# Kernel optimization log

Hardware: AMD Instinct MI355X
Metric: run time of the kernel (lower is better)

The kernel has to match this reference:

```python
import jax, jax.numpy as jnp
import numpy as np

# --- SOM geometry constants (match init_kwargs) ---
MAP_ROWS, MAP_COLS = 32, 32
N_PROTO = MAP_ROWS * MAP_COLS
SIGMA = 1.0
PBC = True


def _build_neighborhood():
    """Gaussian neighborhood h[i,j]=exp(-dist(i,j)^2/(2*sigma^2)) on a hexagonal
    grid with periodic boundary conditions (faithful to Neighborhoods(...,'Hexagons','grid',PBC=True))."""
    rr, cc = np.meshgrid(np.arange(MAP_ROWS), np.arange(MAP_COLS), indexing='ij')
    # hexagonal lattice coordinates: odd rows shifted by 0.5, row spacing sqrt(3)/2
    x = cc + 0.5 * (rr % 2)
    y = rr * (np.sqrt(3.0) / 2.0)
    pos = np.stack([x.ravel(), y.ravel()], axis=1).astype(np.float64)  # [M, 2]
    diff = pos[:, None, :] - pos[None, :, :]                            # [M, M, 2]
    if PBC:
        width = float(MAP_COLS)
        height = MAP_ROWS * (np.sqrt(3.0) / 2.0)
        d2 = np.full((N_PROTO, N_PROTO), np.inf)
        for sx in (-1.0, 0.0, 1.0):
            for sy in (-1.0, 0.0, 1.0):
                dx = diff[..., 0] + sx * width
                dy = diff[..., 1] + sy * height
                d2 = np.minimum(d2, dx * dx + dy * dy)
    else:
        d2 = (diff ** 2).sum(-1)
    return np.exp(-d2 / (2.0 * SIGMA ** 2)).astype(np.float32)         # [M, M]


H = jnp.asarray(_build_neighborhood())  # constant [M, M] neighborhood matrix


def setup_inputs() -> dict:
    key = jax.random.key(0)
    k1, k2 = jax.random.split(key)
    inputs = jax.random.normal(k1, (16384, 256), dtype=jnp.float32)
    prototypes = jax.random.normal(k2, (N_PROTO, 256), dtype=jnp.float32) * 0.05
    return {"inputs": inputs, "prototypes": prototypes}


def reference(inputs, prototypes):
    # squared euclidean distances d[n, m] = ||x_n - p_m||^2, computed without
    # materializing the (N, M, D) broadcast intermediate
    x2 = jnp.sum(inputs * inputs, axis=1, keepdims=True)        # [N, 1]
    p2 = jnp.sum(prototypes * prototypes, axis=1)               # [M]
    d = x2 - 2.0 * (inputs @ prototypes.T) + p2[None, :]        # [N, M]
    energies = H @ d.T                                          # [M, N]
    bmus = jnp.argmin(energies, axis=0)                         # [N]
    out = 0.5 * jnp.take_along_axis(energies, bmus[None, :], axis=0)  # [1, N]
    return out
```

## Files before the change

### kernel.cpp

```cpp
#include <hip/hip_runtime.h>
#include <hip/hip_bf16.h>
#include <math.h>

#define D 256
#define NPROTO 1024
#define NROWS 16384
#define WRr 13
#define WCc 18
#define WJ (WRr * WCc)
#define JSUB 59
#define GMAT_BLOCKS (NPROTO / 4)
#define XPREP_BLOCKS (NROWS / 32)

#define WAITVM(N) asm volatile("s_waitcnt vmcnt(" #N ")" ::: "memory")

typedef __attribute__((ext_vector_type(8))) short short8;
typedef __attribute__((ext_vector_type(4))) float f32x4;

__device__ __forceinline__ int swz_key(int row) {
    return (row & 3) ^ ((row >> 2) & 3);
}

__device__ __forceinline__ short f2bf(float f) {
    union { __hip_bfloat16 b; short s; } u;
    u.b = __float2bfloat16(f);
    return u.s;
}

__device__ __forceinline__ void gload_lds16(void* lds, const void* g) {
    __builtin_amdgcn_global_load_lds(
        (const __attribute__((address_space(1))) unsigned*)g,
        (__attribute__((address_space(3))) unsigned*)lds, 16, 0, 0);
}

__device__ __forceinline__ void proto_pos(int idx, double& x, double& y) {
    int r = idx >> 5, c = idx & 31;
    x = (double)c + 0.5 * (double)(r & 1);
    y = (double)r * 0.86602540378443864676;
}

__device__ __forceinline__ float hval(int i, int j) {
    double xi, yi, xj, yj;
    proto_pos(i, xi, yi);
    proto_pos(j, xj, yj);
    double dx0 = xi - xj, dy0 = yi - yj;
    const double W = 32.0;
    const double Hh = 27.712812921102035;
    double best = 1e300;
#pragma unroll
    for (int sx = -1; sx <= 1; ++sx) {
        double dx = dx0 + (double)sx * W;
#pragma unroll
        for (int sy = -1; sy <= 1; ++sy) {
            double dy = dy0 + (double)sy * Hh;
            double d2 = dx * dx + dy * dy;
            best = fmin(best, d2);
        }
    }
    return (float)exp(-0.5 * best);
}


__global__ void __launch_bounds__(256) prep_kernel(
    const float* __restrict__ X, const float* __restrict__ P,
    short* __restrict__ XgS, short* __restrict__ GbS,
    float* __restrict__ x2, float* __restrict__ hsum, float* __restrict__ hp2,
    unsigned* __restrict__ out) {
    int t = threadIdx.x;
    int bx = blockIdx.x;

    if (bx >= GMAT_BLOCKS) {
        int base0 = (bx - GMAT_BLOCKS) * 32;
        int g = t & 31;
        int kt = g >> 2;
        int slot = g & 3;
#pragma unroll
        for (int it = 0; it < 4; ++it) {
            int row = base0 + it * 8 + (t >> 5);
            const float4* src = reinterpret_cast<const float4*>(X + (size_t)row * D) + g * 2;
            float4 a = src[0], b = src[1];
            float s = a.x * a.x + a.y * a.y + a.z * a.z + a.w * a.w +
                      b.x * b.x + b.y * b.y + b.z * b.z + b.w * b.w;
            s += __shfl_xor(s, 1);
            s += __shfl_xor(s, 2);
            s += __shfl_xor(s, 4);
            s += __shfl_xor(s, 8);
            s += __shfl_xor(s, 16);
            if (g == 0) x2[row] = s;
            short8 w;
            w[0] = f2bf(a.x); w[1] = f2bf(a.y); w[2] = f2bf(a.z); w[3] = f2bf(a.w);
            w[4] = f2bf(b.x); w[5] = f2bf(b.y); w[6] = f2bf(b.z); w[7] = f2bf(b.w);
            *reinterpret_cast<short8*>(
                XgS + (size_t)kt * (NROWS * 32) + (size_t)row * 32 +
                ((slot ^ swz_key(row)) << 3)) = w;
        }
        if (t < 32) out[base0 + t] = 0x7f800000u;
        return;
    }

    __shared__ float ht[4][WJ];
    __shared__ int jrow[WJ];
    __shared__ __align__(16) float gpart[4][4][256];
    __shared__ float hqred[4][4];
    __shared__ float hsred[4][4];
    int i0 = bx * 4;
    int r0 = i0 >> 5, c0 = i0 & 31;

    for (int u = t; u < WJ; u += 256) {
        int jr = (r0 + (u / WCc) - 6 + 32) & 31;
        int jc = (c0 + (u % WCc) - 7 + 32) & 31;
        int j = jr * 32 + jc;
        jrow[u] = j;
#pragma unroll
        for (int s = 0; s < 4; ++s) ht[s][u] = hval(i0 + s, j);
    }
    __syncthreads();

    int w = t >> 6, lane = t & 63;
    int j0 = w * JSUB;
    int j1 = (j0 + JSUB < WJ) ? j0 + JSUB : WJ;
    f32x4 g[4] = {{0.f, 0.f, 0.f, 0.f}, {0.f, 0.f, 0.f, 0.f},
                  {0.f, 0.f, 0.f, 0.f}, {0.f, 0.f, 0.f, 0.f}};
    float hqp[4] = {0.f, 0.f, 0.f, 0.f};
    float hsp[4] = {0.f, 0.f, 0.f, 0.f};
    for (int u = j0; u < j1; ++u) {
        f32x4 pv = *reinterpret_cast<const f32x4*>(P + (size_t)jrow[u] * D + lane * 4);
        float q = pv[0] * pv[0] + pv[1] * pv[1] + pv[2] * pv[2] + pv[3] * pv[3];
#pragma unroll
        for (int s = 0; s < 4; ++s) {
            float h = ht[s][u];
            g[s][0] = fmaf(h, pv[0], g[s][0]);
            g[s][1] = fmaf(h, pv[1], g[s][1]);
            g[s][2] = fmaf(h, pv[2], g[s][2]);
            g[s][3] = fmaf(h, pv[3], g[s][3]);
            hqp[s] = fmaf(h, q, hqp[s]);
            hsp[s] += h;
        }
    }
#pragma unroll
    for (int s = 0; s < 4; ++s)
        *reinterpret_cast<f32x4*>(&gpart[w][s][lane * 4]) = g[s];
#pragma unroll
    for (int s = 0; s < 4; ++s) {
#pragma unroll
        for (int off = 1; off < 64; off <<= 1) hqp[s] += __shfl_xor(hqp[s], off);
    }
    if (lane == 0) {
#pragma unroll
        for (int s = 0; s < 4; ++s) { hqred[w][s] = hqp[s]; hsred[w][s] = hsp[s]; }
    }
    __syncthreads();

    {
        int s = t >> 6;
        f32x4 gs = *reinterpret_cast<const f32x4*>(&gpart[0][s][lane * 4]);
#pragma unroll
        for (int ww = 1; ww < 4; ++ww) {
            f32x4 gp = *reinterpret_cast<const f32x4*>(&gpart[ww][s][lane * 4]);
            gs[0] += gp[0]; gs[1] += gp[1]; gs[2] += gp[2]; gs[3] += gp[3];
        }
        float h0 = __shfl_down(gs[0], 1);
        float h1 = __shfl_down(gs[1], 1);
        float h2 = __shfl_down(gs[2], 1);
        float h3 = __shfl_down(gs[3], 1);
        if (!(lane & 1)) {
            int c = lane >> 1;
            int kt = c >> 2;
            int slot = c & 3;
            int i = i0 + s;
            short8 wv;
            wv[0] = f2bf(gs[0]); wv[1] = f2bf(gs[1]); wv[2] = f2bf(gs[2]); wv[3] = f2bf(gs[3]);
            wv[4] = f2bf(h0);    wv[5] = f2bf(h1);    wv[6] = f2bf(h2);    wv[7] = f2bf(h3);
            *reinterpret_cast<short8*>(
                GbS + (size_t)kt * (NPROTO * 32) + (size_t)i * 32 +
                ((slot ^ swz_key(i)) << 3)) = wv;
        }
    }
    if (t < 4) {
        hsum[i0 + t] = hsred[0][t] + hsred[1][t] + hsred[2][t] + hsred[3][t];
    } else if (t < 8) {
        int s = t - 4;
        hp2[i0 + s] = hqred[0][s] + hqred[1][s] + hqred[2][s] + hqred[3][s];
    }
}

__global__ void __launch_bounds__(256, 4) som8_kernel(
    const short* __restrict__ XgS, const short* __restrict__ GbS,
    const float* __restrict__ x2, const float* __restrict__ hsum,
    const float* __restrict__ hp2, unsigned* __restrict__ out) {
    __shared__ __align__(16) short Xs[2][128 * 32];
    __shared__ __align__(16) short Gs[2][128 * 32];
    __shared__ float red[2][128];

    const int t = threadIdx.x;
    const int lane = t & 63;
    const int wid = t >> 6;
    const int wr = wid >> 1;
    const int wc = wid & 1;
    const int lm = lane & 15;
    const int lq = lane >> 4;
    const int key = (lm & 3) ^ ((lm >> 2) & 3);

    const int lin = blockIdx.x;
    const int w1024 = ((lin & 7) << 7) | (lin >> 3);
    const int n0 = (w1024 >> 3) * 128;
    const int ib0 = (w1024 & 7) * 128;

    f32x4 acc[4][4];
#pragma unroll
    for (int m = 0; m < 4; ++m)
#pragma unroll
        for (int n = 0; n < 4; ++n) acc[m][n] = (f32x4){0.f, 0.f, 0.f, 0.f};

    auto stage = [&](int b, int kt) {
#pragma unroll
        for (int q = 0; q < 2; ++q)
            gload_lds16((char*)(&Xs[b][0]) + q * 4096 + t * 16,
                        XgS + (size_t)kt * (NROWS * 32) +
                        (size_t)(n0 + q * 64 + (t >> 2)) * 32 + ((t & 3) << 3));
#pragma unroll
        for (int q = 0; q < 2; ++q)
            gload_lds16((char*)(&Gs[b][0]) + q * 4096 + t * 16,
                        GbS + (size_t)kt * (NPROTO * 32) +
                        (size_t)(ib0 + q * 64 + (t >> 2)) * 32 + ((t & 3) << 3));
    };

    stage(0, 0);

#pragma unroll
    for (int p = 0; p < 8; ++p) {
        if (p < 7) stage((p + 1) & 1, p + 1);
        if (p < 7) { WAITVM(4); } else { WAITVM(0); }
        __builtin_amdgcn_sched_barrier(0);
        __builtin_amdgcn_s_barrier();

        const short* xb = &Xs[p & 1][0];
        const short* gb = &Gs[p & 1][0];
        const int so = (lq ^ key) << 3;
        short8 a[4], b[4];
#pragma unroll
        for (int m = 0; m < 4; ++m)
            a[m] = *reinterpret_cast<const short8*>(&xb[(wr * 64 + m * 16 + lm) * 32 + so]);
#pragma unroll
        for (int n = 0; n < 4; ++n)
            b[n] = *reinterpret_cast<const short8*>(&gb[(wc * 64 + n * 16 + lm) * 32 + so]);
        __builtin_amdgcn_s_setprio(1);
#pragma unroll
        for (int m = 0; m < 4; ++m)
#pragma unroll
            for (int n = 0; n < 4; ++n)
                acc[m][n] = __builtin_amdgcn_mfma_f32_16x16x32_bf16(a[m], b[n], acc[m][n], 0, 0, 0);
        __builtin_amdgcn_s_setprio(0);
        __builtin_amdgcn_s_barrier();
    }

    float x2v[4][4];
#pragma unroll
    for (int m = 0; m < 4; ++m)
#pragma unroll
        for (int j = 0; j < 4; ++j)
            x2v[m][j] = x2[n0 + wr * 64 + m * 16 + lq * 4 + j];

    float rmin[4][4];
#pragma unroll
    for (int m = 0; m < 4; ++m)
#pragma unroll
        for (int j = 0; j < 4; ++j) rmin[m][j] = 3.4e38f;

#pragma unroll
    for (int ni = 0; ni < 4; ++ni) {
        int ig = ib0 + wc * 64 + ni * 16 + lm;
        float hs = hsum[ig];
        float hq = hp2[ig];
#pragma unroll
        for (int m = 0; m < 4; ++m)
#pragma unroll
            for (int j = 0; j < 4; ++j) {
                float e = fmaf(hs, x2v[m][j], hq) - 2.0f * acc[m][ni][j];
                rmin[m][j] = fminf(rmin[m][j], e);
            }
    }

#pragma unroll
    for (int m = 0; m < 4; ++m)
#pragma unroll
        for (int j = 0; j < 4; ++j) {
            float v = rmin[m][j];
            v = fminf(v, __shfl_xor(v, 1));
            v = fminf(v, __shfl_xor(v, 2));
            v = fminf(v, __shfl_xor(v, 4));
            v = fminf(v, __shfl_xor(v, 8));
            rmin[m][j] = v;
        }
    if (lm == 0) {
#pragma unroll
        for (int m = 0; m < 4; ++m)
#pragma unroll
            for (int j = 0; j < 4; ++j)
                red[wc][wr * 64 + m * 16 + lq * 4 + j] = rmin[m][j];
    }
    __syncthreads();
    if (t < 128) {
        float v = fminf(red[0][t], red[1][t]);
        atomicMin(out + n0 + t, __float_as_uint(0.5f * v));
    }
}

extern "C" void kernel_launch(void* const* d_in, const int* in_sizes, int n_in,
                              void* d_out, int out_size, void* d_ws, size_t ws_size,
                              hipStream_t stream) {
    const float* X = (const float*)d_in[0];
    const float* P = (const float*)d_in[1];
    unsigned* out = (unsigned*)d_out;
    (void)in_sizes; (void)n_in; (void)out_size; (void)ws_size;

    float* ws = (float*)d_ws;
    float* hsum = ws + 1024;
    float* hp2 = ws + 2048;
    float* x2 = ws + 4096;
    short* GbS = (short*)(ws + 32768);
    short* XgS = (short*)(ws + 262144);

    prep_kernel<<<GMAT_BLOCKS + XPREP_BLOCKS, 256, 0, stream>>>(
        X, P, XgS, GbS, x2, hsum, hp2, out);
    som8_kernel<<<1024, 256, 0, stream>>>(XgS, GbS, x2, hsum, hp2, out);
}
```

Before: 32.37 us.

## Fuse input bf16 conversion and row norms into the main GEMM kernel

The separate pass that converted X to swizzled bf16 and computed row squared norms is removed. The main kernel now loads fp32 X rows directly into registers, writes them to an XOR-swizzled fp32 LDS tile, converts to bf16 when building MFMA fragments, and accumulates the row norms on the fly. This drops a full write and re-read of the bf16 copy of X, but doubles LDS use for the X tile, lowers the occupancy hint from 4 to 2 blocks, and repeats the fp32-to-bf16 conversion in each of the 8 prototype-tile blocks that share a row block.

```diff
diff --git a/kernel.cpp b/kernel.cpp
--- a/kernel.cpp
+++ b/kernel.cpp
@@ -10,16 +10,9 @@
 #define WJ (WRr * WCc)
 #define JSUB 59
 #define GMAT_BLOCKS (NPROTO / 4)
-#define XPREP_BLOCKS (NROWS / 32)
-
-#define WAITVM(N) asm volatile("s_waitcnt vmcnt(" #N ")" ::: "memory")
 
 typedef __attribute__((ext_vector_type(8))) short short8;
 typedef __attribute__((ext_vector_type(4))) float f32x4;
-
-__device__ __forceinline__ int swz_key(int row) {
-    return (row & 3) ^ ((row >> 2) & 3);
-}
 
 __device__ __forceinline__ short f2bf(float f) {
     union { __hip_bfloat16 b; short s; } u;
@@ -62,47 +55,19 @@
 
 
 __global__ void __launch_bounds__(256) prep_kernel(
-    const float* __restrict__ X, const float* __restrict__ P,
-    short* __restrict__ XgS, short* __restrict__ GbS,
-    float* __restrict__ x2, float* __restrict__ hsum, float* __restrict__ hp2,
+    const float* __restrict__ P, short* __restrict__ GbS,
+    float* __restrict__ hsum, float* __restrict__ hp2,
     unsigned* __restrict__ out) {
-    int t = threadIdx.x;
-    int bx = blockIdx.x;
-
-    if (bx >= GMAT_BLOCKS) {
-        int base0 = (bx - GMAT_BLOCKS) * 32;
-        int g = t & 31;
-        int kt = g >> 2;
-        int slot = g & 3;
-#pragma unroll
-        for (int it = 0; it < 4; ++it) {
-            int row = base0 + it * 8 + (t >> 5);
-            const float4* src = reinterpret_cast<const float4*>(X + (size_t)row * D) + g * 2;
-            float4 a = src[0], b = src[1];
-            float s = a.x * a.x + a.y * a.y + a.z * a.z + a.w * a.w +
-                      b.x * b.x + b.y * b.y + b.z * b.z + b.w * b.w;
-            s += __shfl_xor(s, 1);
-            s += __shfl_xor(s, 2);
-            s += __shfl_xor(s, 4);
-            s += __shfl_xor(s, 8);
-            s += __shfl_xor(s, 16);
-            if (g == 0) x2[row] = s;
-            short8 w;
-            w[0] = f2bf(a.x); w[1] = f2bf(a.y); w[2] = f2bf(a.z); w[3] = f2bf(a.w);
-            w[4] = f2bf(b.x); w[5] = f2bf(b.y); w[6] = f2bf(b.z); w[7] = f2bf(b.w);
-            *reinterpret_cast<short8*>(
-                XgS + (size_t)kt * (NROWS * 32) + (size_t)row * 32 +
-                ((slot ^ swz_key(row)) << 3)) = w;
-        }
-        if (t < 32) out[base0 + t] = 0x7f800000u;
-        return;
-    }
-
     __shared__ float ht[4][WJ];
     __shared__ int jrow[WJ];
     __shared__ __align__(16) float gpart[4][4][256];
     __shared__ float hqred[4][4];
     __shared__ float hsred[4][4];
+    int t = threadIdx.x;
+    int bx = blockIdx.x;
+
+    if (t < 64) out[bx * 64 + t] = 0x7f800000u;
+
     int i0 = bx * 4;
     int r0 = i0 >> 5, c0 = i0 & 31;
 
@@ -168,12 +133,13 @@
             int kt = c >> 2;
             int slot = c & 3;
             int i = i0 + s;
+            int key = (i & 3) ^ ((i >> 2) & 3);
             short8 wv;
             wv[0] = f2bf(gs[0]); wv[1] = f2bf(gs[1]); wv[2] = f2bf(gs[2]); wv[3] = f2bf(gs[3]);
             wv[4] = f2bf(h0);    wv[5] = f2bf(h1);    wv[6] = f2bf(h2);    wv[7] = f2bf(h3);
             *reinterpret_cast<short8*>(
                 GbS + (size_t)kt * (NPROTO * 32) + (size_t)i * 32 +
-                ((slot ^ swz_key(i)) << 3)) = wv;
+                ((slot ^ key) << 3)) = wv;
         }
     }
     if (t < 4) {
@@ -184,12 +150,13 @@
     }
 }
 
-__global__ void __launch_bounds__(256, 4) som8_kernel(
-    const short* __restrict__ XgS, const short* __restrict__ GbS,
-    const float* __restrict__ x2, const float* __restrict__ hsum,
-    const float* __restrict__ hp2, unsigned* __restrict__ out) {
-    __shared__ __align__(16) short Xs[2][128 * 32];
+__global__ void __launch_bounds__(256, 2) som12_kernel(
+    const float* __restrict__ X, const short* __restrict__ GbS,
+    const float* __restrict__ hsum, const float* __restrict__ hp2,
+    unsigned* __restrict__ out) {
+    __shared__ __align__(16) float Xsf[2][128 * 32];
     __shared__ __align__(16) short Gs[2][128 * 32];
+    __shared__ float x2s[128];
     __shared__ float red[2][128];
 
     const int t = threadIdx.x;
@@ -199,67 +166,107 @@
     const int wc = wid & 1;
     const int lm = lane & 15;
     const int lq = lane >> 4;
-    const int key = (lm & 3) ^ ((lm >> 2) & 3);
-
-    const int lin = blockIdx.x;
-    const int w1024 = ((lin & 7) << 7) | (lin >> 3);
+    const int keyG = (lm & 3) ^ ((lm >> 2) & 3);
+    const int k8 = lm & 7;
+
+    const int bx = blockIdx.x;
+    const int w1024 = ((bx & 7) << 7) | (bx >> 3);
     const int n0 = (w1024 >> 3) * 128;
     const int ib0 = (w1024 & 7) * 128;
 
+    const int srow = t >> 1;
+    const int sh_ = t & 1;
+    const int skey = srow & 7;
+
     f32x4 acc[4][4];
 #pragma unroll
     for (int m = 0; m < 4; ++m)
 #pragma unroll
         for (int n = 0; n < 4; ++n) acc[m][n] = (f32x4){0.f, 0.f, 0.f, 0.f};
 
-    auto stage = [&](int b, int kt) {
-#pragma unroll
-        for (int q = 0; q < 2; ++q)
-            gload_lds16((char*)(&Xs[b][0]) + q * 4096 + t * 16,
-                        XgS + (size_t)kt * (NROWS * 32) +
-                        (size_t)(n0 + q * 64 + (t >> 2)) * 32 + ((t & 3) << 3));
+    float sq = 0.f;
+    f32x4 xr0, xr1, xr2, xr3;
+
+    auto issueX = [&](int kt) {
+        const f32x4* src = reinterpret_cast<const f32x4*>(
+            X + (size_t)(n0 + srow) * D + kt * 32 + sh_ * 16);
+        xr0 = src[0]; xr1 = src[1]; xr2 = src[2]; xr3 = src[3];
+    };
+    auto issueG = [&](int b, int kt) {
 #pragma unroll
         for (int q = 0; q < 2; ++q)
             gload_lds16((char*)(&Gs[b][0]) + q * 4096 + t * 16,
                         GbS + (size_t)kt * (NPROTO * 32) +
                         (size_t)(ib0 + q * 64 + (t >> 2)) * 32 + ((t & 3) << 3));
     };
-
-    stage(0, 0);
-
-#pragma unroll
-    for (int p = 0; p < 8; ++p) {
-        if (p < 7) stage((p + 1) & 1, p + 1);
-        if (p < 7) { WAITVM(4); } else { WAITVM(0); }
-        __builtin_amdgcn_sched_barrier(0);
-        __builtin_amdgcn_s_barrier();
-
-        const short* xb = &Xs[p & 1][0];
-        const short* gb = &Gs[p & 1][0];
-        const int so = (lq ^ key) << 3;
-        short8 a[4], b[4];
+    auto writeX = [&](int b) {
+        char* base = (char*)(&Xsf[b][0]) + srow * 128;
+        *reinterpret_cast<f32x4*>(base + (((sh_ * 4 + 0) ^ skey) << 4)) = xr0;
+        *reinterpret_cast<f32x4*>(base + (((sh_ * 4 + 1) ^ skey) << 4)) = xr1;
+        *reinterpret_cast<f32x4*>(base + (((sh_ * 4 + 2) ^ skey) << 4)) = xr2;
+        *reinterpret_cast<f32x4*>(base + (((sh_ * 4 + 3) ^ skey) << 4)) = xr3;
+        sq += xr0[0] * xr0[0] + xr0[1] * xr0[1] + xr0[2] * xr0[2] + xr0[3] * xr0[3] +
+              xr1[0] * xr1[0] + xr1[1] * xr1[1] + xr1[2] * xr1[2] + xr1[3] * xr1[3] +
+              xr2[0] * xr2[0] + xr2[1] * xr2[1] + xr2[2] * xr2[2] + xr2[3] * xr2[3] +
+              xr3[0] * xr3[0] + xr3[1] * xr3[1] + xr3[2] * xr3[2] + xr3[3] * xr3[3];
+    };
+
+    auto compute = [&](int b) {
+        const char* xbase = (const char*)(&Xsf[b][0]);
+        const short* gb = &Gs[b][0];
+        short8 a[4];
+#pragma unroll
+        for (int m = 0; m < 4; ++m) {
+            int row = wr * 64 + m * 16 + lm;
+            const char* rb = xbase + row * 128;
+            f32x4 lo = *reinterpret_cast<const f32x4*>(rb + ((((lq * 2) + 0) ^ k8) << 4));
+            f32x4 hi = *reinterpret_cast<const f32x4*>(rb + ((((lq * 2) + 1) ^ k8) << 4));
+            short8 av;
+            av[0] = f2bf(lo[0]); av[1] = f2bf(lo[1]); av[2] = f2bf(lo[2]); av[3] = f2bf(lo[3]);
+            av[4] = f2bf(hi[0]); av[5] = f2bf(hi[1]); av[6] = f2bf(hi[2]); av[7] = f2bf(hi[3]);
+            a[m] = av;
+        }
+        short8 b_[4];
+#pragma unroll
+        for (int n = 0; n < 4; ++n)
+            b_[n] = *reinterpret_cast<const short8*>(
+                &gb[(wc * 64 + n * 16 + lm) * 32 + ((lq ^ keyG) << 3)]);
+        __builtin_amdgcn_s_setprio(1);
 #pragma unroll
         for (int m = 0; m < 4; ++m)
-            a[m] = *reinterpret_cast<const short8*>(&xb[(wr * 64 + m * 16 + lm) * 32 + so]);
-#pragma unroll
-        for (int n = 0; n < 4; ++n)
-            b[n] = *reinterpret_cast<const short8*>(&gb[(wc * 64 + n * 16 + lm) * 32 + so]);
-        __builtin_amdgcn_s_setprio(1);
-#pragma unroll
-        for (int m = 0; m < 4; ++m)
 #pragma unroll
             for (int n = 0; n < 4; ++n)
-                acc[m][n] = __builtin_amdgcn_mfma_f32_16x16x32_bf16(a[m], b[n], acc[m][n], 0, 0, 0);
+                acc[m][n] = __builtin_amdgcn_mfma_f32_16x16x32_bf16(a[m], b_[n], acc[m][n], 0, 0, 0);
         __builtin_amdgcn_s_setprio(0);
-        __builtin_amdgcn_s_barrier();
-    }
+    };
+
+    issueG(0, 0);
+    issueX(0);
+    writeX(0);
+    __syncthreads();
+
+#pragma unroll
+    for (int kt = 0; kt < 8; ++kt) {
+        if (kt < 7) {
+            issueG((kt + 1) & 1, kt + 1);
+            issueX(kt + 1);
+        }
+        compute(kt & 1);
+        if (kt < 7) writeX((kt + 1) & 1);
+        __syncthreads();
+    }
+
+    if (sh_ == 0) x2s[srow] = sq;
+    __syncthreads();
+    if (sh_ == 1) x2s[srow] += sq;
+    __syncthreads();
 
     float x2v[4][4];
 #pragma unroll
     for (int m = 0; m < 4; ++m)
 #pragma unroll
         for (int j = 0; j < 4; ++j)
-            x2v[m][j] = x2[n0 + wr * 64 + m * 16 + lq * 4 + j];
+            x2v[m][j] = x2s[wr * 64 + m * 16 + lq * 4 + j];
 
     float rmin[4][4];
 #pragma unroll
@@ -317,11 +324,8 @@
     float* ws = (float*)d_ws;
     float* hsum = ws + 1024;
     float* hp2 = ws + 2048;
-    float* x2 = ws + 4096;
     short* GbS = (short*)(ws + 32768);
-    short* XgS = (short*)(ws + 262144);
-
-    prep_kernel<<<GMAT_BLOCKS + XPREP_BLOCKS, 256, 0, stream>>>(
-        X, P, XgS, GbS, x2, hsum, hp2, out);
-    som8_kernel<<<1024, 256, 0, stream>>>(XgS, GbS, x2, hsum, hp2, out);
-}
+
+    prep_kernel<<<GMAT_BLOCKS, 256, 0, stream>>>(P, GbS, hsum, hp2, out);
+    som12_kernel<<<1024, 256, 0, stream>>>(X, GbS, hsum, hp2, out);
+}
```

Measured after the change: 36.93 us. 1.14x slower.
